# Optimization experiments

Hardware: AMD Instinct MI355X
Metric: run time of the kernel (lower is better)

## Reference

```python
import jax, jax.numpy as jnp
import numpy as np

N_NODES = 100000
N_EDGES = 800000
F_IN, N_HID, N_CLS = 256, 128, 40


def setup_inputs() -> dict:
    key = jax.random.key(0)
    ks = jax.random.split(key, 6)
    features = jax.random.normal(ks[0], (N_NODES, F_IN), dtype=jnp.float32)
    src = jax.random.randint(ks[1], (N_EDGES,), 0, N_NODES, dtype=jnp.int64)
    dst = jax.random.randint(ks[2], (N_EDGES,), 0, N_NODES, dtype=jnp.int64)
    W1 = jax.random.normal(ks[3], (F_IN, N_HID), dtype=jnp.float32) / np.sqrt(F_IN)
    b1 = jnp.zeros((N_HID,), dtype=jnp.float32)
    W2 = jax.random.normal(ks[4], (N_HID, N_CLS), dtype=jnp.float32) / np.sqrt(N_HID)
    b2 = jnp.zeros((N_CLS,), dtype=jnp.float32)
    return {"features": features, "src": src, "dst": dst,
            "W1": W1, "b1": b1, "W2": W2, "b2": b2}


def reference(features, src, dst, W1, b1, W2, b2):
    # DGL GraphConv with norm='both': h = D_dst^{-1/2} A (D_src^{-1/2} x) W + b
    # Eval mode: dropout(p=0.85) is identity.
    N = features.shape[0]
    ones = jnp.ones(src.shape[0], dtype=features.dtype)
    out_deg = jax.ops.segment_sum(ones, src, num_segments=N)
    in_deg = jax.ops.segment_sum(ones, dst, num_segments=N)
    norm_src = jnp.where(out_deg > 0, out_deg ** -0.5, 0.0)[:, None]  # [N,1]
    norm_dst = jnp.where(in_deg > 0, in_deg ** -0.5, 0.0)[:, None]

    def gconv(x, W, b):
        # project first (in_feats >= out_feats here) to shrink SpMM width
        h = (x * norm_src) @ W                                # [N, out]
        agg = jax.ops.segment_sum(h[src], dst, num_segments=N)  # sparse aggregate
        return agg * norm_dst + b

    x = jax.nn.relu(gconv(features, W1, b1))
    return gconv(x, W2, b2)
```

## Files before the change

kernel.cpp:

```cpp
#include <hip/hip_runtime.h>
#include <hip/hip_bf16.h>
#include <math.h>


#define F_IN  256
#define F_HID 128
#define F_CLS 40

#define RSZ 8192
#define NSL 32

typedef __bf16 bf16_t;
typedef bf16_t bf16x8 __attribute__((ext_vector_type(8)));
typedef float floatx4 __attribute__((ext_vector_type(4)));
typedef _Float16 f16x8 __attribute__((ext_vector_type(8)));

static __device__ __forceinline__ unsigned short f2b(float f) {
    __hip_bfloat16 h = __float2bfloat16(f);
    return __builtin_bit_cast(unsigned short, h);
}
static __device__ __forceinline__ float b2f(unsigned short u) {
    return __uint_as_float((unsigned)u << 16);
}
static __device__ __forceinline__ unsigned short f2h(float f) {
    return __builtin_bit_cast(unsigned short, (_Float16)f);
}
static __device__ __forceinline__ float h2f(unsigned short u) {
    return (float)__builtin_bit_cast(_Float16, u);
}

__global__ __launch_bounds__(256) void hist_kernel(
    const int* __restrict__ src, const int* __restrict__ dst,
    unsigned* __restrict__ partial_s, unsigned* __restrict__ partial_d, int E)
{
    __shared__ unsigned h[RSZ];
    const int t = threadIdx.x;
    const int r  = blockIdx.x / NSL;
    const int sl = blockIdx.x % NSL;
    const int lo = r * RSZ;
    const int* __restrict__ keys = blockIdx.y ? dst : src;
    unsigned* __restrict__ part = blockIdx.y ? partial_d : partial_s;

    for (int i = t; i < RSZ; i += 256) h[i] = 0;
    __syncthreads();

    const int slice = (E + NSL - 1) / NSL;
    const int e0 = sl * slice;
    const int e1 = min(E, e0 + slice);

    int e = e0 + t;
    for (; e + 7 * 256 < e1; e += 8 * 256) {
        int k[8];
        #pragma unroll
        for (int i = 0; i < 8; ++i) k[i] = keys[e + i * 256];
        #pragma unroll
        for (int i = 0; i < 8; ++i) {
            unsigned kk = (unsigned)(k[i] - lo);
            if (kk < RSZ) atomicAdd(&h[kk], 1u);
        }
    }
    for (; e < e1; e += 256) {
        unsigned kk = (unsigned)(keys[e] - lo);
        if (kk < RSZ) atomicAdd(&h[kk], 1u);
    }
    __syncthreads();

    unsigned* dst_p = part + (size_t)blockIdx.x * RSZ;
    for (int i = t; i < RSZ; i += 256) dst_p[i] = h[i];
}

__global__ __launch_bounds__(256) void scan1_kernel(
    const unsigned* __restrict__ partial_s, const unsigned* __restrict__ partial_d,
    int* __restrict__ row_off, int* __restrict__ blk_sums,
    float* __restrict__ norm_src, float* __restrict__ norm_dst, int N)
{
    __shared__ int s[256];
    const int t = threadIdx.x;
    const int base = blockIdx.x * 1024 + t * 4;

    unsigned ss0 = 0, ss1 = 0, ss2 = 0, ss3 = 0;
    unsigned sd0 = 0, sd1 = 0, sd2 = 0, sd3 = 0;
    {
        const int r = base / RSZ;
        const int off = base & (RSZ - 1);
        const unsigned* ps = partial_s + (size_t)r * NSL * RSZ + off;
        const unsigned* pd = partial_d + (size_t)r * NSL * RSZ + off;
        #pragma unroll
        for (int sl = 0; sl < NSL; ++sl) {
            uint4 a = *(const uint4*)(ps + (size_t)sl * RSZ);
            uint4 b = *(const uint4*)(pd + (size_t)sl * RSZ);
            ss0 += a.x; ss1 += a.y; ss2 += a.z; ss3 += a.w;
            sd0 += b.x; sd1 += b.y; sd2 += b.z; sd3 += b.w;
        }
    }
    if (base + 0 < N) {
        norm_src[base + 0] = ss0 ? 1.0f / sqrtf((float)ss0) : 0.0f;
        norm_dst[base + 0] = sd0 ? 1.0f / sqrtf((float)sd0) : 0.0f;
    }
    if (base + 1 < N) {
        norm_src[base + 1] = ss1 ? 1.0f / sqrtf((float)ss1) : 0.0f;
        norm_dst[base + 1] = sd1 ? 1.0f / sqrtf((float)sd1) : 0.0f;
    }
    if (base + 2 < N) {
        norm_src[base + 2] = ss2 ? 1.0f / sqrtf((float)ss2) : 0.0f;
        norm_dst[base + 2] = sd2 ? 1.0f / sqrtf((float)sd2) : 0.0f;
    }
    if (base + 3 < N) {
        norm_src[base + 3] = ss3 ? 1.0f / sqrtf((float)ss3) : 0.0f;
        norm_dst[base + 3] = sd3 ? 1.0f / sqrtf((float)sd3) : 0.0f;
    }

    int v0 = (base + 0 < N) ? (int)sd0 : 0;
    int v1 = (base + 1 < N) ? (int)sd1 : 0;
    int v2 = (base + 2 < N) ? (int)sd2 : 0;
    int v3 = (base + 3 < N) ? (int)sd3 : 0;
    int local = v0 + v1 + v2 + v3;
    s[t] = local;
    __syncthreads();
    for (int off = 1; off < 256; off <<= 1) {
        int x = (t >= off) ? s[t - off] : 0;
        __syncthreads();
        s[t] += x;
        __syncthreads();
    }
    int excl = s[t] - local;
    if (t == 255) blk_sums[blockIdx.x] = s[t];
    if (base + 0 < N) row_off[base + 0] = excl;
    if (base + 1 < N) row_off[base + 1] = excl + v0;
    if (base + 2 < N) row_off[base + 2] = excl + v0 + v1;
    if (base + 3 < N) row_off[base + 3] = excl + v0 + v1 + v2;
}

__global__ __launch_bounds__(256) void scan2_pack_kernel(
    int* __restrict__ blk_sums, int B,
    const float* __restrict__ W1, __hip_bfloat16* __restrict__ W1t,
    const float* __restrict__ W2, unsigned short* __restrict__ W2t)
{
    const int t = threadIdx.x;
    if (blockIdx.x > 128) {
        int idx = (blockIdx.x - 129) * 256 + t;
        int n = idx >> 7;
        int k = idx & 127;
        W2t[idx] = (n < F_CLS) ? f2h(W2[(size_t)k * F_CLS + n]) : (unsigned short)0;
        return;
    }
    if (blockIdx.x > 0) {
        int idx = (blockIdx.x - 1) * 256 + t;
        int n = idx >> 8;
        int k = idx & 255;
        W1t[idx] = __float2bfloat16(W1[(size_t)k * F_HID + n]);
        return;
    }
    __shared__ int s[256];
    int local = (t < B) ? blk_sums[t] : 0;
    s[t] = local;
    __syncthreads();
    for (int off = 1; off < 256; off <<= 1) {
        int x = (t >= off) ? s[t - off] : 0;
        __syncthreads();
        s[t] += x;
        __syncthreads();
    }
    if (t < B) blk_sums[t] = s[t] - local;
}

__global__ __launch_bounds__(256) void scan3_slicepref_kernel(
    int* __restrict__ row_off, const int* __restrict__ blk_sums,
    unsigned* __restrict__ partial_d, int N, int E, int NRtot)
{
    const int idx = blockIdx.x * 256 + threadIdx.x;
    if (idx >= NRtot) return;
    unsigned run = 0;
    if (idx < N) {
        int v = row_off[idx] + blk_sums[idx >> 10];
        row_off[idx] = v;
        run = (unsigned)v;
    }
    if (idx == N) row_off[N] = E;
    const int r = idx / RSZ;
    const int i = idx & (RSZ - 1);
    unsigned* p = partial_d + (size_t)r * NSL * RSZ + i;
    #pragma unroll
    for (int sl = 0; sl < NSL; ++sl) {
        unsigned c = p[(size_t)sl * RSZ];
        p[(size_t)sl * RSZ] = run;
        run += c;
    }
}

__global__ __launch_bounds__(256) void scatter2_kernel(
    const int* __restrict__ src, const int* __restrict__ dst,
    const unsigned* __restrict__ pref, int* __restrict__ csr_src, int E)
{
    __shared__ unsigned cur[RSZ];
    const int t = threadIdx.x;
    const int r  = blockIdx.x / NSL;
    const int sl = blockIdx.x % NSL;
    const int lo = r * RSZ;
    const unsigned* p = pref + (size_t)blockIdx.x * RSZ;

    for (int i = t; i < RSZ; i += 256) cur[i] = p[i];
    __syncthreads();

    const int slice = (E + NSL - 1) / NSL;
    const int e0 = sl * slice;
    const int e1 = min(E, e0 + slice);

    int e = e0 + t;
    for (; e + 7 * 256 < e1; e += 8 * 256) {
        int d[8], s[8];
        #pragma unroll
        for (int i = 0; i < 8; ++i) { d[i] = dst[e + i * 256]; s[i] = src[e + i * 256]; }
        #pragma unroll
        for (int i = 0; i < 8; ++i) {
            unsigned k = (unsigned)(d[i] - lo);
            if (k < RSZ) {
                unsigned pos = atomicAdd(&cur[k], 1u);
                csr_src[pos] = s[i];
            }
        }
    }
    for (; e < e1; e += 256) {
        unsigned k = (unsigned)(dst[e] - lo);
        if (k < RSZ) {
            unsigned pos = atomicAdd(&cur[k], 1u);
            csr_src[pos] = src[e];
        }
    }
}

__global__ __launch_bounds__(512, 4) void gemm1_mfma_kernel(
    const float* __restrict__ X, const __hip_bfloat16* __restrict__ W1t,
    const float* __restrict__ norm_src, __hip_bfloat16* __restrict__ h1b, int N)
{
    __shared__ __hip_bfloat16 Bs[128 * 256];
    const int t = threadIdx.x;
    const int node0 = blockIdx.x * 128;
    const int lane = t & 63;
    const int w = t >> 6;
    const int l15 = lane & 15;
    const int quad = lane >> 4;

    const int arow = node0 + w * 16 + l15;
    const int arow_c = (arow < N) ? arow : (N - 1);
    const float* xp = X + (size_t)arow_c * F_IN + quad * 8;

    float4 ar[2][4];
    ar[0][0] = *(const float4*)(xp + 0);
    ar[0][1] = *(const float4*)(xp + 4);
    ar[0][2] = *(const float4*)(xp + 32);
    ar[0][3] = *(const float4*)(xp + 36);
    ar[1][0] = *(const float4*)(xp + 64 + 0);
    ar[1][1] = *(const float4*)(xp + 64 + 4);
    ar[1][2] = *(const float4*)(xp + 64 + 32);
    ar[1][3] = *(const float4*)(xp + 64 + 36);

    #pragma unroll
    for (int i = 0; i < 8; ++i) {
        int idx = i * 512 + t;
        int row = idx >> 5;
        int ch  = idx & 31;
        uint4 v = *(const uint4*)(W1t + (size_t)row * F_IN + ch * 8);
        int d = row * 256 + ((ch * 8) ^ ((row & 7) << 3));
        *(uint4*)(Bs + d) = v;
    }
    __syncthreads();

    const int swz = (l15 & 7) << 3;
    const int bbase0 = l15 * 256 + ((quad * 8) ^ swz);
    const int bbase1 = l15 * 256 + ((32 + quad * 8) ^ swz);

    floatx4 acc[8] = {};

    #pragma unroll
    for (int c = 0; c < 4; ++c) {
        const int p = c & 1;
        bf16x8 ab0, ab1;
        {
            union { bf16x8 v; unsigned short u[8]; } cv;
            cv.u[0] = f2b(ar[p][0].x); cv.u[1] = f2b(ar[p][0].y);
            cv.u[2] = f2b(ar[p][0].z); cv.u[3] = f2b(ar[p][0].w);
            cv.u[4] = f2b(ar[p][1].x); cv.u[5] = f2b(ar[p][1].y);
            cv.u[6] = f2b(ar[p][1].z); cv.u[7] = f2b(ar[p][1].w);
            ab0 = cv.v;
            cv.u[0] = f2b(ar[p][2].x); cv.u[1] = f2b(ar[p][2].y);
            cv.u[2] = f2b(ar[p][2].z); cv.u[3] = f2b(ar[p][2].w);
            cv.u[4] = f2b(ar[p][3].x); cv.u[5] = f2b(ar[p][3].y);
            cv.u[6] = f2b(ar[p][3].z); cv.u[7] = f2b(ar[p][3].w);
            ab1 = cv.v;
        }
        if (c < 2) {
            ar[p][0] = *(const float4*)(xp + (c + 2) * 64 + 0);
            ar[p][1] = *(const float4*)(xp + (c + 2) * 64 + 4);
            ar[p][2] = *(const float4*)(xp + (c + 2) * 64 + 32);
            ar[p][3] = *(const float4*)(xp + (c + 2) * 64 + 36);
        }
        #pragma unroll
        for (int nt = 0; nt < 8; ++nt) {
            bf16x8 b = *(const bf16x8*)(Bs + bbase0 + nt * 16 * 256 + c * 64);
            acc[nt] = __builtin_amdgcn_mfma_f32_16x16x32_bf16(ab0, b, acc[nt], 0, 0, 0);
        }
        #pragma unroll
        for (int nt = 0; nt < 8; ++nt) {
            bf16x8 b = *(const bf16x8*)(Bs + bbase1 + nt * 16 * 256 + c * 64);
            acc[nt] = __builtin_amdgcn_mfma_f32_16x16x32_bf16(ab1, b, acc[nt], 0, 0, 0);
        }
    }

    #pragma unroll
    for (int r = 0; r < 4; ++r) {
        int node = node0 + w * 16 + quad * 4 + r;
        if (node < N) {
            float ns = norm_src[node];
            #pragma unroll
            for (int nt = 0; nt < 8; ++nt)
                h1b[(size_t)node * F_HID + nt * 16 + l15] =
                    __float2bfloat16(acc[nt][r] * ns);
        }
    }
}

__global__ __launch_bounds__(512) void spmm1_fused_kernel(
    const __hip_bfloat16* __restrict__ h1b, const int* __restrict__ row_off,
    const int* __restrict__ csr_src, const float* __restrict__ norm_src,
    const float* __restrict__ norm_dst, const float* __restrict__ b1,
    const unsigned short* __restrict__ W2t, unsigned short* __restrict__ h2, int N)
{
    __shared__ unsigned short As[16][136];
    const int t = threadIdx.x;
    const int g = t >> 5;
    const int node = blockIdx.x * 16 + g;
    const int c = (t & 31) << 2;

    if (node < N) {
        const int start = row_off[node];
        const int end = row_off[node + 1];
        float4 acc = make_float4(0.f, 0.f, 0.f, 0.f);
        int j = start;
        for (; j + 8 <= end; j += 8) {
            int s[8];
            #pragma unroll
            for (int i = 0; i < 8; ++i) s[i] = csr_src[j + i];
            ushort4 u[8];
            #pragma unroll
            for (int i = 0; i < 8; ++i)
                u[i] = *(const ushort4*)(h1b + (size_t)s[i] * F_HID + c);
            #pragma unroll
            for (int i = 0; i < 8; ++i) {
                acc.x += b2f(u[i].x);
                acc.y += b2f(u[i].y);
                acc.z += b2f(u[i].z);
                acc.w += b2f(u[i].w);
            }
        }
        for (; j + 2 <= end; j += 2) {
            int s0 = csr_src[j + 0];
            int s1 = csr_src[j + 1];
            ushort4 u0 = *(const ushort4*)(h1b + (size_t)s0 * F_HID + c);
            ushort4 u1 = *(const ushort4*)(h1b + (size_t)s1 * F_HID + c);
            acc.x += b2f(u0.x) + b2f(u1.x);
            acc.y += b2f(u0.y) + b2f(u1.y);
            acc.z += b2f(u0.z) + b2f(u1.z);
            acc.w += b2f(u0.w) + b2f(u1.w);
        }
        if (j < end) {
            int s = csr_src[j];
            ushort4 u = *(const ushort4*)(h1b + (size_t)s * F_HID + c);
            acc.x += b2f(u.x);
            acc.y += b2f(u.y);
            acc.z += b2f(u.z);
            acc.w += b2f(u.w);
        }
        const float nd = norm_dst[node];
        const float ns = norm_src[node];
        float4 bb = *(const float4*)(b1 + c);
        ushort4 o;
        o.x = f2h(fmaxf(fmaf(acc.x, nd, bb.x), 0.f) * ns);
        o.y = f2h(fmaxf(fmaf(acc.y, nd, bb.y), 0.f) * ns);
        o.z = f2h(fmaxf(fmaf(acc.z, nd, bb.z), 0.f) * ns);
        o.w = f2h(fmaxf(fmaf(acc.w, nd, bb.w), 0.f) * ns);
        *(ushort4*)&As[g][c] = o;
    } else {
        ushort4 z = make_ushort4(0, 0, 0, 0);
        *(ushort4*)&As[g][c] = z;
    }
    __syncthreads();
    if (t >= 64) return;

    const int l15 = t & 15;
    const int quad = t >> 4;
    floatx4 co[3] = {};
    #pragma unroll
    for (int kc = 0; kc < 4; ++kc) {
        f16x8 a = *(const f16x8*)&As[l15][kc * 32 + quad * 8];
        #pragma unroll
        for (int ct = 0; ct < 3; ++ct) {
            f16x8 b = *(const f16x8*)(W2t + (size_t)(ct * 16 + l15) * F_HID
                                          + kc * 32 + quad * 8);
            co[ct] = __builtin_amdgcn_mfma_f32_16x16x32_f16(a, b, co[ct], 0, 0, 0);
        }
    }
    const int node0 = blockIdx.x * 16;
    #pragma unroll
    for (int ct = 0; ct < 3; ++ct) {
        int col = ct * 16 + l15;
        if (col < F_CLS) {
            #pragma unroll
            for (int i = 0; i < 4; ++i) {
                int n2 = node0 + quad * 4 + i;
                if (n2 < N) h2[(size_t)n2 * F_CLS + col] = f2h(co[ct][i]);
            }
        }
    }
}

__global__ __launch_bounds__(256) void spmm2_csr_kernel(
    const unsigned short* __restrict__ h2, const int* __restrict__ row_off,
    const int* __restrict__ csr_src, const float* __restrict__ norm_dst,
    const float* __restrict__ b2, float* __restrict__ out, int N)
{
    const int t = threadIdx.x;
    if (t >= 250) return;
    const int node = blockIdx.x * 25 + t / 10;
    const int lane = t % 10;
    if (node >= N) return;
    const int c = lane << 2;
    const int start = row_off[node];
    const int end = row_off[node + 1];
    float4 acc = make_float4(0.f, 0.f, 0.f, 0.f);
    int j = start;
    for (; j + 8 <= end; j += 8) {
        int s[8];
        #pragma unroll
        for (int i = 0; i < 8; ++i) s[i] = csr_src[j + i];
        ushort4 u[8];
        #pragma unroll
        for (int i = 0; i < 8; ++i)
            u[i] = *(const ushort4*)(h2 + (size_t)s[i] * F_CLS + c);
        #pragma unroll
        for (int i = 0; i < 8; ++i) {
            acc.x += h2f(u[i].x);
            acc.y += h2f(u[i].y);
            acc.z += h2f(u[i].z);
            acc.w += h2f(u[i].w);
        }
    }
    for (; j + 2 <= end; j += 2) {
        int s0 = csr_src[j + 0];
        int s1 = csr_src[j + 1];
        ushort4 u0 = *(const ushort4*)(h2 + (size_t)s0 * F_CLS + c);
        ushort4 u1 = *(const ushort4*)(h2 + (size_t)s1 * F_CLS + c);
        acc.x += h2f(u0.x) + h2f(u1.x);
        acc.y += h2f(u0.y) + h2f(u1.y);
        acc.z += h2f(u0.z) + h2f(u1.z);
        acc.w += h2f(u0.w) + h2f(u1.w);
    }
    if (j < end) {
        int s = csr_src[j];
        ushort4 u = *(const ushort4*)(h2 + (size_t)s * F_CLS + c);
        acc.x += h2f(u.x);
        acc.y += h2f(u.y);
        acc.z += h2f(u.z);
        acc.w += h2f(u.w);
    }
    float nd = norm_dst[node];
    float4 bb = *(const float4*)(b2 + c);
    float4 r;
    r.x = fmaf(acc.x, nd, bb.x);
    r.y = fmaf(acc.y, nd, bb.y);
    r.z = fmaf(acc.z, nd, bb.z);
    r.w = fmaf(acc.w, nd, bb.w);
    *(float4*)(out + (size_t)node * F_CLS + c) = r;
}

extern "C" void kernel_launch(void* const* d_in, const int* in_sizes, int n_in,
                              void* d_out, int out_size, void* d_ws, size_t ws_size,
                              hipStream_t stream) {
    const float* X   = (const float*)d_in[0];
    const int*   src = (const int*)d_in[1];
    const int*   dst = (const int*)d_in[2];
    const float* W1  = (const float*)d_in[3];
    const float* b1  = (const float*)d_in[4];
    const float* W2  = (const float*)d_in[5];
    const float* b2  = (const float*)d_in[6];
    float* out = (float*)d_out;

    const int N = in_sizes[0] / F_IN;
    const int E = in_sizes[1];
    const int NB = (N + 1023) / 1024;
    const int NR = (N + RSZ - 1) / RSZ;
    const int NRtot = NR * RSZ;

    char* w = (char*)d_ws;
    int*   row_off  = (int*)w;                      w += (size_t)(N + 4) * 4;
    int*   blk_sums = (int*)w;                      w += 256 * 4;
    int*   csr_src  = (int*)w;                      w += (size_t)E * 4;
    float* norm_src = (float*)w;                    w += (size_t)N * 4;
    float* norm_dst = (float*)w;                    w += (size_t)N * 4;
    unsigned short* h2 = (unsigned short*)w;        w += (size_t)N * F_CLS * 2;
    __hip_bfloat16* W1t = (__hip_bfloat16*)w;       w += (size_t)F_HID * F_IN * 2;
    unsigned short* W2t = (unsigned short*)w;       w += (size_t)48 * F_HID * 2;
    __hip_bfloat16* h1b = (__hip_bfloat16*)w;       w += (size_t)N * F_HID * 2;
    unsigned* partial_s = (unsigned*)w;             w += (size_t)NR * NSL * RSZ * 4;
    unsigned* partial_d = (unsigned*)w;             w += (size_t)NR * NSL * RSZ * 4;

    hist_kernel<<<dim3(NR * NSL, 2), 256, 0, stream>>>(src, dst, partial_s, partial_d, E);

    scan1_kernel<<<NB, 256, 0, stream>>>(partial_s, partial_d, row_off, blk_sums,
                                         norm_src, norm_dst, N);
    scan2_pack_kernel<<<153, 256, 0, stream>>>(blk_sums, NB, W1, W1t, W2, W2t);
    scan3_slicepref_kernel<<<(NRtot + 255) / 256, 256, 0, stream>>>(
        row_off, blk_sums, partial_d, N, E, NRtot);

    scatter2_kernel<<<NR * NSL, 256, 0, stream>>>(src, dst, partial_d, csr_src, E);

    gemm1_mfma_kernel<<<(N + 127) / 128, 512, 0, stream>>>(X, W1t, norm_src, h1b, N);

    spmm1_fused_kernel<<<(N + 15) / 16, 512, 0, stream>>>(h1b, row_off, csr_src,
                                                          norm_src, norm_dst, b1,
                                                          W2t, h2, N);

    spmm2_csr_kernel<<<(N + 24) / 25, 256, 0, stream>>>(h2, row_off, csr_src,
                                                        norm_dst, b2, out, N);
}
```

Measured before the change: 300.5 us.

## Fuse degree histogram into GEMM1 launch and move src-norm scaling into SpMM

The degree histogram blocks are merged into the GEMM1 launch as extra blocks, so the memory-bound histogram work can run alongside the compute-bound projection. This requires GEMM1 to no longer depend on norm_src, so the source-degree scaling moves into the first SpMM as a per-edge fmaf with a gathered norm_src value. The weight packing gets its own kernel that runs first, and the block-sum scan becomes a standalone kernel. In exchange the SpMM does an extra random 4-byte gather per edge, and the histogram blocks inherit the GEMM's 64 KB shared-memory footprint and 512-thread shape.

New measurement: 311.9 us. 1.04x slower.

```diff
diff --git a/kernel.cpp b/kernel.cpp
--- a/kernel.cpp
+++ b/kernel.cpp
@@ -29,212 +29,75 @@
     return (float)__builtin_bit_cast(_Float16, u);
 }
 
-__global__ __launch_bounds__(256) void hist_kernel(
-    const int* __restrict__ src, const int* __restrict__ dst,
-    unsigned* __restrict__ partial_s, unsigned* __restrict__ partial_d, int E)
-{
-    __shared__ unsigned h[RSZ];
-    const int t = threadIdx.x;
-    const int r  = blockIdx.x / NSL;
-    const int sl = blockIdx.x % NSL;
-    const int lo = r * RSZ;
-    const int* __restrict__ keys = blockIdx.y ? dst : src;
-    unsigned* __restrict__ part = blockIdx.y ? partial_d : partial_s;
-
-    for (int i = t; i < RSZ; i += 256) h[i] = 0;
-    __syncthreads();
-
-    const int slice = (E + NSL - 1) / NSL;
-    const int e0 = sl * slice;
-    const int e1 = min(E, e0 + slice);
-
-    int e = e0 + t;
-    for (; e + 7 * 256 < e1; e += 8 * 256) {
-        int k[8];
-        #pragma unroll
-        for (int i = 0; i < 8; ++i) k[i] = keys[e + i * 256];
-        #pragma unroll
-        for (int i = 0; i < 8; ++i) {
-            unsigned kk = (unsigned)(k[i] - lo);
-            if (kk < RSZ) atomicAdd(&h[kk], 1u);
-        }
-    }
-    for (; e < e1; e += 256) {
-        unsigned kk = (unsigned)(keys[e] - lo);
-        if (kk < RSZ) atomicAdd(&h[kk], 1u);
-    }
-    __syncthreads();
-
-    unsigned* dst_p = part + (size_t)blockIdx.x * RSZ;
-    for (int i = t; i < RSZ; i += 256) dst_p[i] = h[i];
-}
-
-__global__ __launch_bounds__(256) void scan1_kernel(
-    const unsigned* __restrict__ partial_s, const unsigned* __restrict__ partial_d,
-    int* __restrict__ row_off, int* __restrict__ blk_sums,
-    float* __restrict__ norm_src, float* __restrict__ norm_dst, int N)
-{
-    __shared__ int s[256];
-    const int t = threadIdx.x;
-    const int base = blockIdx.x * 1024 + t * 4;
-
-    unsigned ss0 = 0, ss1 = 0, ss2 = 0, ss3 = 0;
-    unsigned sd0 = 0, sd1 = 0, sd2 = 0, sd3 = 0;
-    {
-        const int r = base / RSZ;
-        const int off = base & (RSZ - 1);
-        const unsigned* ps = partial_s + (size_t)r * NSL * RSZ + off;
-        const unsigned* pd = partial_d + (size_t)r * NSL * RSZ + off;
-        #pragma unroll
-        for (int sl = 0; sl < NSL; ++sl) {
-            uint4 a = *(const uint4*)(ps + (size_t)sl * RSZ);
-            uint4 b = *(const uint4*)(pd + (size_t)sl * RSZ);
-            ss0 += a.x; ss1 += a.y; ss2 += a.z; ss3 += a.w;
-            sd0 += b.x; sd1 += b.y; sd2 += b.z; sd3 += b.w;
-        }
-    }
-    if (base + 0 < N) {
-        norm_src[base + 0] = ss0 ? 1.0f / sqrtf((float)ss0) : 0.0f;
-        norm_dst[base + 0] = sd0 ? 1.0f / sqrtf((float)sd0) : 0.0f;
-    }
-    if (base + 1 < N) {
-        norm_src[base + 1] = ss1 ? 1.0f / sqrtf((float)ss1) : 0.0f;
-        norm_dst[base + 1] = sd1 ? 1.0f / sqrtf((float)sd1) : 0.0f;
-    }
-    if (base + 2 < N) {
-        norm_src[base + 2] = ss2 ? 1.0f / sqrtf((float)ss2) : 0.0f;
-        norm_dst[base + 2] = sd2 ? 1.0f / sqrtf((float)sd2) : 0.0f;
-    }
-    if (base + 3 < N) {
-        norm_src[base + 3] = ss3 ? 1.0f / sqrtf((float)ss3) : 0.0f;
-        norm_dst[base + 3] = sd3 ? 1.0f / sqrtf((float)sd3) : 0.0f;
-    }
-
-    int v0 = (base + 0 < N) ? (int)sd0 : 0;
-    int v1 = (base + 1 < N) ? (int)sd1 : 0;
-    int v2 = (base + 2 < N) ? (int)sd2 : 0;
-    int v3 = (base + 3 < N) ? (int)sd3 : 0;
-    int local = v0 + v1 + v2 + v3;
-    s[t] = local;
-    __syncthreads();
-    for (int off = 1; off < 256; off <<= 1) {
-        int x = (t >= off) ? s[t - off] : 0;
-        __syncthreads();
-        s[t] += x;
-        __syncthreads();
-    }
-    int excl = s[t] - local;
-    if (t == 255) blk_sums[blockIdx.x] = s[t];
-    if (base + 0 < N) row_off[base + 0] = excl;
-    if (base + 1 < N) row_off[base + 1] = excl + v0;
-    if (base + 2 < N) row_off[base + 2] = excl + v0 + v1;
-    if (base + 3 < N) row_off[base + 3] = excl + v0 + v1 + v2;
-}
-
-__global__ __launch_bounds__(256) void scan2_pack_kernel(
-    int* __restrict__ blk_sums, int B,
+__global__ __launch_bounds__(256) void pack_kernel(
     const float* __restrict__ W1, __hip_bfloat16* __restrict__ W1t,
     const float* __restrict__ W2, unsigned short* __restrict__ W2t)
 {
     const int t = threadIdx.x;
-    if (blockIdx.x > 128) {
-        int idx = (blockIdx.x - 129) * 256 + t;
+    if (blockIdx.x < 128) {
+        int idx = blockIdx.x * 256 + t;
+        int n = idx >> 8;
+        int k = idx & 255;
+        W1t[idx] = __float2bfloat16(W1[(size_t)k * F_HID + n]);
+    } else {
+        int idx = (blockIdx.x - 128) * 256 + t;
         int n = idx >> 7;
         int k = idx & 127;
         W2t[idx] = (n < F_CLS) ? f2h(W2[(size_t)k * F_CLS + n]) : (unsigned short)0;
+    }
+}
+
+__global__ __launch_bounds__(512, 4) void fused_gemm1_hist_kernel(
+    const float* __restrict__ X, const __hip_bfloat16* __restrict__ W1t,
+    __hip_bfloat16* __restrict__ h1b, int N, int G,
+    const int* __restrict__ src, const int* __restrict__ dst,
+    unsigned* __restrict__ partial_s, unsigned* __restrict__ partial_d, int E)
+{
+    __shared__ __align__(16) unsigned char smem[65536];
+    const int t = threadIdx.x;
+
+    if ((int)blockIdx.x >= G) {
+        unsigned* h = (unsigned*)smem;
+        const int hb = blockIdx.x - G;
+        const int y  = hb / (NSL * ((N + RSZ - 1) / RSZ));
+        const int rb = hb % (NSL * ((N + RSZ - 1) / RSZ));
+        const int r  = rb / NSL;
+        const int sl = rb % NSL;
+        const int lo = r * RSZ;
+        const int* __restrict__ keys = y ? dst : src;
+        unsigned* __restrict__ part = y ? partial_d : partial_s;
+
+        for (int i = t; i < RSZ; i += 512) h[i] = 0;
+        __syncthreads();
+
+        const int slice = (E + NSL - 1) / NSL;
+        const int e0 = sl * slice;
+        const int e1 = min(E, e0 + slice);
+
+        int e = e0 + t;
+        for (; e + 7 * 512 < e1; e += 8 * 512) {
+            int k[8];
+            #pragma unroll
+            for (int i = 0; i < 8; ++i) k[i] = keys[e + i * 512];
+            #pragma unroll
+            for (int i = 0; i < 8; ++i) {
+                unsigned kk = (unsigned)(k[i] - lo);
+                if (kk < RSZ) atomicAdd(&h[kk], 1u);
+            }
+        }
+        for (; e < e1; e += 512) {
+            unsigned kk = (unsigned)(keys[e] - lo);
+            if (kk < RSZ) atomicAdd(&h[kk], 1u);
+        }
+        __syncthreads();
+
+        unsigned* dst_p = part + (size_t)rb * RSZ + (size_t)y * 0;
+        dst_p = part + (size_t)rb * RSZ;
+        for (int i = t; i < RSZ; i += 512) dst_p[i] = h[i];
         return;
     }
-    if (blockIdx.x > 0) {
-        int idx = (blockIdx.x - 1) * 256 + t;
-        int n = idx >> 8;
-        int k = idx & 255;
-        W1t[idx] = __float2bfloat16(W1[(size_t)k * F_HID + n]);
-        return;
-    }
-    __shared__ int s[256];
-    int local = (t < B) ? blk_sums[t] : 0;
-    s[t] = local;
-    __syncthreads();
-    for (int off = 1; off < 256; off <<= 1) {
-        int x = (t >= off) ? s[t - off] : 0;
-        __syncthreads();
-        s[t] += x;
-        __syncthreads();
-    }
-    if (t < B) blk_sums[t] = s[t] - local;
-}
-
-__global__ __launch_bounds__(256) void scan3_slicepref_kernel(
-    int* __restrict__ row_off, const int* __restrict__ blk_sums,
-    unsigned* __restrict__ partial_d, int N, int E, int NRtot)
-{
-    const int idx = blockIdx.x * 256 + threadIdx.x;
-    if (idx >= NRtot) return;
-    unsigned run = 0;
-    if (idx < N) {
-        int v = row_off[idx] + blk_sums[idx >> 10];
-        row_off[idx] = v;
-        run = (unsigned)v;
-    }
-    if (idx == N) row_off[N] = E;
-    const int r = idx / RSZ;
-    const int i = idx & (RSZ - 1);
-    unsigned* p = partial_d + (size_t)r * NSL * RSZ + i;
-    #pragma unroll
-    for (int sl = 0; sl < NSL; ++sl) {
-        unsigned c = p[(size_t)sl * RSZ];
-        p[(size_t)sl * RSZ] = run;
-        run += c;
-    }
-}
-
-__global__ __launch_bounds__(256) void scatter2_kernel(
-    const int* __restrict__ src, const int* __restrict__ dst,
-    const unsigned* __restrict__ pref, int* __restrict__ csr_src, int E)
-{
-    __shared__ unsigned cur[RSZ];
-    const int t = threadIdx.x;
-    const int r  = blockIdx.x / NSL;
-    const int sl = blockIdx.x % NSL;
-    const int lo = r * RSZ;
-    const unsigned* p = pref + (size_t)blockIdx.x * RSZ;
-
-    for (int i = t; i < RSZ; i += 256) cur[i] = p[i];
-    __syncthreads();
-
-    const int slice = (E + NSL - 1) / NSL;
-    const int e0 = sl * slice;
-    const int e1 = min(E, e0 + slice);
-
-    int e = e0 + t;
-    for (; e + 7 * 256 < e1; e += 8 * 256) {
-        int d[8], s[8];
-        #pragma unroll
-        for (int i = 0; i < 8; ++i) { d[i] = dst[e + i * 256]; s[i] = src[e + i * 256]; }
-        #pragma unroll
-        for (int i = 0; i < 8; ++i) {
-            unsigned k = (unsigned)(d[i] - lo);
-            if (k < RSZ) {
-                unsigned pos = atomicAdd(&cur[k], 1u);
-                csr_src[pos] = s[i];
-            }
-        }
-    }
-    for (; e < e1; e += 256) {
-        unsigned k = (unsigned)(dst[e] - lo);
-        if (k < RSZ) {
-            unsigned pos = atomicAdd(&cur[k], 1u);
-            csr_src[pos] = src[e];
-        }
-    }
-}
-
-__global__ __launch_bounds__(512, 4) void gemm1_mfma_kernel(
-    const float* __restrict__ X, const __hip_bfloat16* __restrict__ W1t,
-    const float* __restrict__ norm_src, __hip_bfloat16* __restrict__ h1b, int N)
-{
-    __shared__ __hip_bfloat16 Bs[128 * 256];
-    const int t = threadIdx.x;
+
+    __hip_bfloat16* Bs = (__hip_bfloat16*)smem;
     const int node0 = blockIdx.x * 128;
     const int lane = t & 63;
     const int w = t >> 6;
@@ -311,11 +174,152 @@
     for (int r = 0; r < 4; ++r) {
         int node = node0 + w * 16 + quad * 4 + r;
         if (node < N) {
-            float ns = norm_src[node];
             #pragma unroll
             for (int nt = 0; nt < 8; ++nt)
                 h1b[(size_t)node * F_HID + nt * 16 + l15] =
-                    __float2bfloat16(acc[nt][r] * ns);
+                    __float2bfloat16(acc[nt][r]);
+        }
+    }
+}
+
+__global__ __launch_bounds__(256) void scan1_kernel(
+    const unsigned* __restrict__ partial_s, const unsigned* __restrict__ partial_d,
+    int* __restrict__ row_off, int* __restrict__ blk_sums,
+    float* __restrict__ norm_src, float* __restrict__ norm_dst, int N)
+{
+    __shared__ int s[256];
+    const int t = threadIdx.x;
+    const int base = blockIdx.x * 1024 + t * 4;
+
+    unsigned ss0 = 0, ss1 = 0, ss2 = 0, ss3 = 0;
+    unsigned sd0 = 0, sd1 = 0, sd2 = 0, sd3 = 0;
+    {
+        const int r = base / RSZ;
+        const int off = base & (RSZ - 1);
+        const unsigned* ps = partial_s + (size_t)r * NSL * RSZ + off;
+        const unsigned* pd = partial_d + (size_t)r * NSL * RSZ + off;
+        #pragma unroll
+        for (int sl = 0; sl < NSL; ++sl) {
+            uint4 a = *(const uint4*)(ps + (size_t)sl * RSZ);
+            uint4 b = *(const uint4*)(pd + (size_t)sl * RSZ);
+            ss0 += a.x; ss1 += a.y; ss2 += a.z; ss3 += a.w;
+            sd0 += b.x; sd1 += b.y; sd2 += b.z; sd3 += b.w;
+        }
+    }
+    if (base + 0 < N) {
+        norm_src[base + 0] = ss0 ? 1.0f / sqrtf((float)ss0) : 0.0f;
+        norm_dst[base + 0] = sd0 ? 1.0f / sqrtf((float)sd0) : 0.0f;
+    }
+    if (base + 1 < N) {
+        norm_src[base + 1] = ss1 ? 1.0f / sqrtf((float)ss1) : 0.0f;
+        norm_dst[base + 1] = sd1 ? 1.0f / sqrtf((float)sd1) : 0.0f;
+    }
+    if (base + 2 < N) {
+        norm_src[base + 2] = ss2 ? 1.0f / sqrtf((float)ss2) : 0.0f;
+        norm_dst[base + 2] = sd2 ? 1.0f / sqrtf((float)sd2) : 0.0f;
+    }
+    if (base + 3 < N) {
+        norm_src[base + 3] = ss3 ? 1.0f / sqrtf((float)ss3) : 0.0f;
+        norm_dst[base + 3] = sd3 ? 1.0f / sqrtf((float)sd3) : 0.0f;
+    }
+
+    int v0 = (base + 0 < N) ? (int)sd0 : 0;
+    int v1 = (base + 1 < N) ? (int)sd1 : 0;
+    int v2 = (base + 2 < N) ? (int)sd2 : 0;
+    int v3 = (base + 3 < N) ? (int)sd3 : 0;
+    int local = v0 + v1 + v2 + v3;
+    s[t] = local;
+    __syncthreads();
+    for (int off = 1; off < 256; off <<= 1) {
+        int x = (t >= off) ? s[t - off] : 0;
+        __syncthreads();
+        s[t] += x;
+        __syncthreads();
+    }
+    int excl = s[t] - local;
+    if (t == 255) blk_sums[blockIdx.x] = s[t];
+    if (base + 0 < N) row_off[base + 0] = excl;
+    if (base + 1 < N) row_off[base + 1] = excl + v0;
+    if (base + 2 < N) row_off[base + 2] = excl + v0 + v1;
+    if (base + 3 < N) row_off[base + 3] = excl + v0 + v1 + v2;
+}
+
+__global__ __launch_bounds__(256) void scan2_kernel(int* __restrict__ blk_sums, int B) {
+    __shared__ int s[256];
+    const int t = threadIdx.x;
+    int local = (t < B) ? blk_sums[t] : 0;
+    s[t] = local;
+    __syncthreads();
+    for (int off = 1; off < 256; off <<= 1) {
+        int x = (t >= off) ? s[t - off] : 0;
+        __syncthreads();
+        s[t] += x;
+        __syncthreads();
+    }
+    if (t < B) blk_sums[t] = s[t] - local;
+}
+
+__global__ __launch_bounds__(256) void scan3_slicepref_kernel(
+    int* __restrict__ row_off, const int* __restrict__ blk_sums,
+    unsigned* __restrict__ partial_d, int N, int E, int NRtot)
+{
+    const int idx = blockIdx.x * 256 + threadIdx.x;
+    if (idx >= NRtot) return;
+    unsigned run = 0;
+    if (idx < N) {
+        int v = row_off[idx] + blk_sums[idx >> 10];
+        row_off[idx] = v;
+        run = (unsigned)v;
+    }
+    if (idx == N) row_off[N] = E;
+    const int r = idx / RSZ;
+    const int i = idx & (RSZ - 1);
+    unsigned* p = partial_d + (size_t)r * NSL * RSZ + i;
+    #pragma unroll
+    for (int sl = 0; sl < NSL; ++sl) {
+        unsigned c = p[(size_t)sl * RSZ];
+        p[(size_t)sl * RSZ] = run;
+        run += c;
+    }
+}
+
+__global__ __launch_bounds__(256) void scatter2_kernel(
+    const int* __restrict__ src, const int* __restrict__ dst,
+    const unsigned* __restrict__ pref, int* __restrict__ csr_src, int E)
+{
+    __shared__ unsigned cur[RSZ];
+    const int t = threadIdx.x;
+    const int r  = blockIdx.x / NSL;
+    const int sl = blockIdx.x % NSL;
+    const int lo = r * RSZ;
+    const unsigned* p = pref + (size_t)blockIdx.x * RSZ;
+
+    for (int i = t; i < RSZ; i += 256) cur[i] = p[i];
+    __syncthreads();
+
+    const int slice = (E + NSL - 1) / NSL;
+    const int e0 = sl * slice;
+    const int e1 = min(E, e0 + slice);
+
+    int e = e0 + t;
+    for (; e + 7 * 256 < e1; e += 8 * 256) {
+        int d[8], s[8];
+        #pragma unroll
+        for (int i = 0; i < 8; ++i) { d[i] = dst[e + i * 256]; s[i] = src[e + i * 256]; }
+        #pragma unroll
+        for (int i = 0; i < 8; ++i) {
+            unsigned k = (unsigned)(d[i] - lo);
+            if (k < RSZ) {
+                unsigned pos = atomicAdd(&cur[k], 1u);
+                csr_src[pos] = s[i];
+            }
+        }
+    }
+    for (; e < e1; e += 256) {
+        unsigned k = (unsigned)(dst[e] - lo);
+        if (k < RSZ) {
+            unsigned pos = atomicAdd(&cur[k], 1u);
+            csr_src[pos] = src[e];
         }
     }
 }
@@ -342,34 +346,28 @@
             #pragma unroll
             for (int i = 0; i < 8; ++i) s[i] = csr_src[j + i];
             ushort4 u[8];
-            #pragma unroll
-            for (int i = 0; i < 8; ++i)
+            float nsv[8];
+            #pragma unroll
+            for (int i = 0; i < 8; ++i) {
                 u[i] = *(const ushort4*)(h1b + (size_t)s[i] * F_HID + c);
+                nsv[i] = norm_src[s[i]];
+            }
             #pragma unroll
             for (int i = 0; i < 8; ++i) {
-                acc.x += b2f(u[i].x);
-                acc.y += b2f(u[i].y);
-                acc.z += b2f(u[i].z);
-                acc.w += b2f(u[i].w);
+                acc.x = fmaf(b2f(u[i].x), nsv[i], acc.x);
+                acc.y = fmaf(b2f(u[i].y), nsv[i], acc.y);
+                acc.z = fmaf(b2f(u[i].z), nsv[i], acc.z);
+                acc.w = fmaf(b2f(u[i].w), nsv[i], acc.w);
             }
         }
-        for (; j + 2 <= end; j += 2) {
-            int s0 = csr_src[j + 0];
-            int s1 = csr_src[j + 1];
-            ushort4 u0 = *(const ushort4*)(h1b + (size_t)s0 * F_HID + c);
-            ushort4 u1 = *(const ushort4*)(h1b + (size_t)s1 * F_HID + c);
-            acc.x += b2f(u0.x) + b2f(u1.x);
-            acc.y += b2f(u0.y) + b2f(u1.y);
-            acc.z += b2f(u0.z) + b2f(u1.z);
-            acc.w += b2f(u0.w) + b2f(u1.w);
-        }
-        if (j < end) {
+        for (; j < end; ++j) {
             int s = csr_src[j];
+            float nsv = norm_src[s];
             ushort4 u = *(const ushort4*)(h1b + (size_t)s * F_HID + c);
-            acc.x += b2f(u.x);
-            acc.y += b2f(u.y);
-            acc.z += b2f(u.z);
-            acc.w += b2f(u.w);
+            acc.x = fmaf(b2f(u.x), nsv, acc.x);
+            acc.y = fmaf(b2f(u.y), nsv, acc.y);
+            acc.z = fmaf(b2f(u.z), nsv, acc.z);
+            acc.w = fmaf(b2f(u.w), nsv, acc.w);
         }
         const float nd = norm_dst[node];
         const float ns = norm_src[node];
@@ -490,6 +488,8 @@
     const int NB = (N + 1023) / 1024;
     const int NR = (N + RSZ - 1) / RSZ;
     const int NRtot = NR * RSZ;
+    const int G  = (N + 127) / 128;
+    const int HB = NR * NSL * 2;
 
     char* w = (char*)d_ws;
     int*   row_off  = (int*)w;                      w += (size_t)(N + 4) * 4;
@@ -504,17 +504,18 @@
     unsigned* partial_s = (unsigned*)w;             w += (size_t)NR * NSL * RSZ * 4;
     unsigned* partial_d = (unsigned*)w;             w += (size_t)NR * NSL * RSZ * 4;
 
-    hist_kernel<<<dim3(NR * NSL, 2), 256, 0, stream>>>(src, dst, partial_s, partial_d, E);
+    pack_kernel<<<152, 256, 0, stream>>>(W1, W1t, W2, W2t);
+
+    fused_gemm1_hist_kernel<<<G + HB, 512, 0, stream>>>(
+        X, W1t, h1b, N, G, src, dst, partial_s, partial_d, E);
 
     scan1_kernel<<<NB, 256, 0, stream>>>(partial_s, partial_d, row_off, blk_sums,
                                          norm_src, norm_dst, N);
-    scan2_pack_kernel<<<153, 256, 0, stream>>>(blk_sums, NB, W1, W1t, W2, W2t);
+    scan2_kernel<<<1, 256, 0, stream>>>(blk_sums, NB);
     scan3_slicepref_kernel<<<(NRtot + 255) / 256, 256, 0, stream>>>(
         row_off, blk_sums, partial_d, N, E, NRtot);
 
     scatter2_kernel<<<NR * NSL, 256, 0, stream>>>(src, dst, partial_d, csr_src, E);
-
-    gemm1_mfma_kernel<<<(N + 127) / 128, 512, 0, stream>>>(X, W1t, norm_src, h1b, N);
 
     spmm1_fused_kernel<<<(N + 15) / 16, 512, 0, stream>>>(h1b, row_off, csr_src,
                                                           norm_src, norm_dst, b1,
```
